# Kernel tuning notes

Hardware: AMD Instinct MI355X
Metric: run time of the kernel (lower is better)

The kernel has to match this reference:

```python
import jax, jax.numpy as jnp
import numpy as np

# ---- static architecture config (mirrors DynamicNetwork/MixedBlock) ----
B = 8192          # batch
ND = 13           # num dense feats
NS = 26           # num sparse feats
D = 16            # embedding_dim
VPF = 50000       # vocab per sparse field
VOCAB = ND + NS * VPF
BIN = 400         # block_in_dim
BOUT = 400        # block_out_dim
NB = 4            # num blocks
K = 4             # num candidate block types
REG = 1e-5        # weights_reg
# binarized one-hot arch choices (weights.data one-hot per segment in original)
CH1 = [0, 1, 1, 1]        # chosen prev node for input 1 of block i
CH2 = [1, 2, 3, 4]        # chosen prev node for input 2 of block i
CHK = [i % K for i in range(NB)]  # chosen candidate block type
OFFS = ND + VPF * np.arange(NS, dtype=np.int64)  # sparse field offsets


def _one_hot_alpha(n_prev, i1, i2, k):
    a = np.zeros(2 * n_prev + K, dtype=np.float32)
    a[i1] = 1.0
    a[n_prev + i2] = 1.0
    a[2 * n_prev + k] = 1.0
    return jnp.asarray(a)


def setup_inputs() -> dict:
    key = jax.random.key(0)
    ks = jax.random.split(key, 12)
    raw_dense = jax.random.uniform(ks[0], (B, ND), dtype=jnp.float32)
    raw_sparse = jax.random.randint(ks[1], (B, NS), 0, VPF, dtype=jnp.int64)
    emb_table = jax.random.normal(ks[2], (VOCAB, D), dtype=jnp.float32) * 0.01
    P_dense = jax.random.normal(ks[3], (ND * D, BIN), dtype=jnp.float32) * 0.02
    P_sparse = jax.random.normal(ks[4], (NS * D, BIN), dtype=jnp.float32) * 0.02
    P_block = jax.random.normal(ks[5], (BOUT, BIN), dtype=jnp.float32) * 0.02
    Wc = jax.random.normal(ks[6], (NB, K, BIN, BOUT), dtype=jnp.float32) * 0.02
    bc = jnp.zeros((NB, K, BOUT), dtype=jnp.float32)
    clf_w = jax.random.normal(ks[7], (NB * BOUT, 1), dtype=jnp.float32) * 0.02
    clf_b = jnp.zeros((1,), dtype=jnp.float32)
    alphas = {f'a{i}': _one_hot_alpha(2 + i, CH1[i], CH2[i], CHK[i]) for i in range(NB)}
    return dict(raw_dense=raw_dense, raw_sparse=raw_sparse, emb_table=emb_table,
                P_dense=P_dense, P_sparse=P_sparse, P_block=P_block,
                Wc=Wc, bc=bc, clf_w=clf_w, clf_b=clf_b, **alphas)


def _forward(raw_dense, raw_sparse, emb_table, P_dense, P_sparse, P_block,
             Wc, bc, clf_w, clf_b, alphas):
    # init node 1: dense embedding scaled by raw dense values -> [B, ND*D]
    dense_emb = emb_table[:ND][None, :, :] * raw_dense[:, :, None]
    # init node 2: sparse embedding lookup with field offsets -> [B, NS*D]
    sparse_idx = raw_sparse + jnp.asarray(OFFS)[None, :]
    sparse_emb = emb_table[sparse_idx]
    nodes = [dense_emb.reshape(B, ND * D), sparse_emb.reshape(B, NS * D)]
    projs = [P_dense, P_sparse]
    norms = jnp.linalg.norm(dense_emb) + jnp.linalg.norm(sparse_emb)
    for i in range(NB):
        n_prev = 2 + i
        a = alphas[i]
        seg1, seg2, segc = a[:n_prev], a[n_prev:2 * n_prev], a[-K:]
        i1, i2, kk = CH1[i], CH2[i], CHK[i]
        # masked weighted sum: chosen node scaled by its (one) weight; zero
        # weights enter additively as scalars (faithful to `else w` branch)
        x1 = seg1[i1] * nodes[i1] + (seg1.sum() - seg1[i1])
        x2 = seg2[i2] * nodes[i2] + (seg2.sum() - seg2[i2])
        # candidate block (MLP): type-specific input projection + ReLU + linear
        h = jax.nn.relu(x1 @ projs[i1] + x2 @ projs[i2])  # [B, BIN]
        out_k = h @ Wc[i, kk] + bc[i, kk]                 # [B, BOUT]
        node = segc[kk] * out_k + (segc.sum() - segc[kk])
        nodes.append(node)
        projs.append(P_block)
    output = jnp.concatenate(nodes[2:], axis=1)  # [B, NB*BOUT]
    logits = output @ clf_w + clf_b              # [B, 1]
    regs = REG * norms
    return logits, regs


def reference(raw_dense, raw_sparse, emb_table, P_dense, P_sparse, P_block,
              Wc, bc, clf_w, clf_b, a0, a1, a2, a3):
    return _forward(raw_dense, raw_sparse, emb_table, P_dense, P_sparse,
                    P_block, Wc, bc, clf_w, clf_b, [a0, a1, a2, a3])
```

## Files before the change

### kernel.cpp

```cpp
#include <hip/hip_runtime.h>
#include <cstddef>


typedef short short8 __attribute__((ext_vector_type(8)));
typedef float floatx16 __attribute__((ext_vector_type(16)));

#define EMB_BLOCKS 832

__device__ __forceinline__ unsigned short f2bf(float f) {
    unsigned int u = __float_as_uint(f);
    u += 0x7fffu + ((u >> 16) & 1u);
    return (unsigned short)(u >> 16);
}
__device__ __forceinline__ float bf2f(unsigned short h) {
    return __uint_as_float((unsigned int)h << 16);
}
__device__ __forceinline__ void split2(float v, unsigned short& h, unsigned short& l) {
    h = f2bf(v);
    l = f2bf(v - bf2f(h));
}

__global__ __launch_bounds__(256) void prep1_kernel(
    const float* __restrict__ Pd, const float* __restrict__ Ps, const float* __restrict__ Pb,
    const float* __restrict__ a0, const float* __restrict__ a1,
    const float* __restrict__ a2, const float* __restrict__ a3,
    float* __restrict__ scal,
    float* __restrict__ csd, float* __restrict__ css, float* __restrict__ csb)
{
    int t = threadIdx.x;
    int y = blockIdx.y;
    int c = t & 31, rg = t >> 5;
    int col = blockIdx.x * 32 + c;
    const float* src = (y==0) ? Pd : (y==1) ? Ps : Pb;
    int K = (y==0) ? 208 : (y==1) ? 416 : 400;
    float* out = (y==0) ? csd : (y==1) ? css : csb;
    float s = 0.f;
    if (col < 400)
        for (int k = rg; k < K; k += 8) s += src[(size_t)k*400 + col];
    __shared__ float red[8][32];
    red[rg][c] = s;
    __syncthreads();
    if (rg == 0 && col < 400) {
        float tot = 0.f;
        #pragma unroll
        for (int r = 0; r < 8; ++r) tot += red[r][c];
        out[col] = tot;
    }
    if (blockIdx.x == 0 && y == 0 && t < 4) {
        int i = t;
        const float* a = (i==0) ? a0 : (i==1) ? a1 : (i==2) ? a2 : a3;
        int np = 2 + i;
        float sum1 = 0.f, sum2 = 0.f, sumc = 0.f;
        for (int j = 0; j < np; ++j) { sum1 += a[j]; sum2 += a[np+j]; }
        for (int j = 0; j < 4; ++j) sumc += a[2*np+j];
        int i1 = (i==0) ? 0 : 1;
        int i2 = i + 1;
        int kk = i;
        float s1 = a[i1],      c1 = sum1 - s1;
        float s2 = a[np+i2],   c2 = sum2 - s2;
        float sk = a[2*np+kk], ck = sumc - sk;
        float* sl = scal + i*8;
        if (i == 0) { sl[0]=s1; sl[1]=c1; sl[2]=s2; sl[3]=c2; }
        else        { sl[0]=s2; sl[1]=c2; sl[2]=s1; sl[3]=c1; }
        sl[4] = sk; sl[5] = ck;
    }
}

__global__ __launch_bounds__(256) void prep2_kernel(
    const float* __restrict__ Pd, const float* __restrict__ Ps,
    const float* __restrict__ scal,
    unsigned short* __restrict__ w0, unsigned short* __restrict__ ws)
{
    int z = blockIdx.z;
    int Kp = (z==0) ? 208 : 416;
    const float* src = (z==0) ? Pd : Ps;
    unsigned short* dst = (z==0) ? w0 : ws;
    size_t plo = (size_t)512 * Kp;

    int ktiles = (Kp + 63) >> 6;
    if ((int)blockIdx.y >= ktiles) return;
    float sc = (z==0) ? scal[0] : 1.f;
    int k0 = blockIdx.y * 64, n0 = blockIdx.x * 64;
    __shared__ float T[64][65];
    int t = threadIdx.x;
    {
        int kr = t >> 2, c0 = (t & 3) * 16;
        int gk = k0 + kr;
        bool kok = gk < Kp;
        for (int j = 0; j < 16; j += 4) {
            int n = n0 + c0 + j;
            float4 v = make_float4(0.f,0.f,0.f,0.f);
            if (kok && n < 400) v = *(const float4*)&src[(size_t)gk*400 + n];
            T[kr][c0+j+0] = v.x * sc;
            T[kr][c0+j+1] = v.y * sc;
            T[kr][c0+j+2] = v.z * sc;
            T[kr][c0+j+3] = v.w * sc;
        }
    }
    __syncthreads();
    {
        int nr = t >> 2, kc0 = (t & 3) * 16;
        int gn = n0 + nr;
        int gk0 = k0 + kc0;
        if (gk0 >= Kp) return;
        unsigned short hb[16], lb[16];
        for (int j = 0; j < 16; ++j) {
            float v = (gn < 400) ? T[kc0+j][nr] : 0.f;
            split2(v, hb[j], lb[j]);
        }
        int kb = gk0 >> 4;
        size_t off = (((size_t)kb*16 + (gn>>5))*64 + (gn&31))*8;
        *(uint4*)&dst[off]             = *(uint4*)&hb[0];
        *(uint4*)&dst[off + 256]       = *(uint4*)&hb[8];
        *(uint4*)&dst[plo + off]       = *(uint4*)&lb[0];
        *(uint4*)&dst[plo + off + 256] = *(uint4*)&lb[8];
    }
}

__global__ __launch_bounds__(256) void prepM_kernel(
    const float* __restrict__ Wc, const float* __restrict__ Pb,
    const float* __restrict__ scal,
    unsigned short* __restrict__ w1, unsigned short* __restrict__ w2,
    unsigned short* __restrict__ w3)
{
    int z = blockIdx.z;
    unsigned short* dst = (z==0) ? w1 : (z==1) ? w2 : w3;
    const float* A = Wc + (size_t)z*5*160000;
    float scale = scal[(z+1)*8+0] * scal[z*8+4];
    const size_t plo = (size_t)512*400;

    __shared__ float As[16][68];
    __shared__ float Ws[16][68];
    int t = threadIdx.x;
    int tx = t & 15, ty = t >> 4;
    int bk = blockIdx.y * 64;
    int bn = blockIdx.x * 64;
    int arow = t >> 2;
    int aj4  = (t & 3) << 2;
    int wrow = t >> 4;
    int wc4  = (t & 15) << 2;
    float acc[4][4] = {};
    for (int j0 = 0; j0 < 400; j0 += 16) {
        float4 av = make_float4(0.f,0.f,0.f,0.f);
        if (bk + arow < 400) av = *(const float4*)&A[(size_t)(bk+arow)*400 + j0 + aj4];
        float4 wv = make_float4(0.f,0.f,0.f,0.f);
        if (bn + wc4 < 400) wv = *(const float4*)&Pb[(size_t)(j0+wrow)*400 + bn + wc4];
        __syncthreads();
        As[aj4+0][arow] = av.x;
        As[aj4+1][arow] = av.y;
        As[aj4+2][arow] = av.z;
        As[aj4+3][arow] = av.w;
        *(float4*)&Ws[wrow][wc4] = wv;
        __syncthreads();
        #pragma unroll
        for (int jj = 0; jj < 16; ++jj) {
            float4 a4 = *(const float4*)&As[jj][ty<<2];
            float4 b4 = *(const float4*)&Ws[jj][tx<<2];
            acc[0][0] += a4.x*b4.x; acc[0][1] += a4.x*b4.y; acc[0][2] += a4.x*b4.z; acc[0][3] += a4.x*b4.w;
            acc[1][0] += a4.y*b4.x; acc[1][1] += a4.y*b4.y; acc[1][2] += a4.y*b4.z; acc[1][3] += a4.y*b4.w;
            acc[2][0] += a4.z*b4.x; acc[2][1] += a4.z*b4.y; acc[2][2] += a4.z*b4.z; acc[2][3] += a4.z*b4.w;
            acc[3][0] += a4.w*b4.x; acc[3][1] += a4.w*b4.y; acc[3][2] += a4.w*b4.z; acc[3][3] += a4.w*b4.w;
        }
    }
    int gk0 = bk + (ty << 2);
    int gn0 = bn + (tx << 2);
    #pragma unroll
    for (int ik = 0; ik < 4; ++ik) {
        int gk = gk0 + ik;
        if (gk >= 400) break;
        int kb = gk >> 4, hh8 = (gk >> 3) & 1, e = gk & 7;
        #pragma unroll
        for (int in = 0; in < 4; ++in) {
            int gn = gn0 + in;
            float v = (gn < 400) ? acc[ik][in] * scale : 0.f;
            unsigned short h16, l16; split2(v, h16, l16);
            size_t off = (((size_t)kb*16 + (gn>>5))*64 + hh8*32 + (gn&31))*8 + e;
            dst[off] = h16;
            dst[plo + off] = l16;
        }
    }
}

__global__ __launch_bounds__(256) void prepvec_kernel(
    const float* __restrict__ scal,
    const float* __restrict__ csd, const float* __restrict__ css, const float* __restrict__ csb,
    const float* __restrict__ Wc, const float* __restrict__ bc,
    const float* __restrict__ clf_w, const float* __restrict__ Pb,
    float* __restrict__ cv, float* __restrict__ gv, float* __restrict__ scl2)
{
    int i = blockIdx.y;
    int tid = threadIdx.x;
    int tbase = blockIdx.x * 32;
    const float* cw = clf_w + i*400;
    float ski = scal[i*8+4], cki = scal[i*8+5];
    const float* A = Wc + (size_t)i*5*160000;

    int wv = tid >> 6, lane = tid & 63;
    #pragma unroll
    for (int q = 0; q < 8; ++q) {
        int t = tbase + wv*8 + q;
        float s = 0.f;
        if (t < 400) {
            const float* wr = A + (size_t)t*400;
            for (int j = lane; j < 400; j += 64) s += wr[j]*cw[j];
            #pragma unroll
            for (int o = 32; o > 0; o >>= 1) s += __shfl_xor(s, o);
        }
        if (lane == 0) gv[i*448 + t] = (t < 400) ? ski * s : 0.f;
    }

    __shared__ float bpred[8][32];
    int t = tbase + (tid & 31);
    int jc = tid >> 5;
    float bp_part = 0.f;
    if (i > 0 && t < 400) {
        const float* bcp = bc + (size_t)(i-1)*5*400;
        for (int j = jc*50; j < jc*50 + 50; ++j)
            bp_part += bcp[j] * Pb[(size_t)j*400 + t];
    }
    bpred[jc][tid & 31] = bp_part;
    __syncthreads();
    if (tid < 32) {
        float bp = 0.f;
        #pragma unroll
        for (int r = 0; r < 8; ++r) bp += bpred[r][tid];
        float c = 0.f;
        if (t < 400) {
            if (i == 0) {
                c = scal[1]*csd[t] + scal[3]*css[t];
            } else {
                float s2 = scal[i*8+0], c2 = scal[i*8+1];
                float c1 = scal[i*8+3];
                float skp = scal[(i-1)*8+4], ckp = scal[(i-1)*8+5];
                c = c1*css[t] + (c2 + s2*ckp)*csb[t] + s2*skp*bp;
            }
        }
        cv[i*448 + t] = c;
    }

    if (blockIdx.x == 0) {
        const float* bci = bc + (size_t)i*5*400;
        float sc = 0.f;
        for (int j = tid; j < 400; j += 256) sc += (ski*bci[j] + cki)*cw[j];
        #pragma unroll
        for (int o = 32; o > 0; o >>= 1) sc += __shfl_down(sc, o);
        __shared__ float red[4];
        int wv2 = tid >> 6, ln = tid & 63;
        if (ln == 0) red[wv2] = sc;
        __syncthreads();
        if (tid == 0) scl2[i] = red[0]+red[1]+red[2]+red[3];
    }
}

__global__ __launch_bounds__(256) void embed_kernel(
    const float* __restrict__ rd, const int* __restrict__ rs,
    const float* __restrict__ emb,
    unsigned short* __restrict__ n0h, unsigned short* __restrict__ n0l,
    unsigned short* __restrict__ n1h, unsigned short* __restrict__ n1l,
    float* __restrict__ partial)
{
    int tid0 = blockIdx.x*256 + threadIdx.x;
    int nth = gridDim.x*256;
    float ssq = 0.f, dsq = 0.f;
    for (int it = tid0; it < 8192*26; it += nth) {
        int s = it >> 13, b = it & 8191;
        int row = 13 + 50000*s + rs[b*26 + s];
        const float* e = emb + (size_t)row*16;
        float4 e0 = *(const float4*)&e[0], e1 = *(const float4*)&e[4];
        float4 e2 = *(const float4*)&e[8], e3 = *(const float4*)&e[12];
        float vv[16] = {e0.x,e0.y,e0.z,e0.w, e1.x,e1.y,e1.z,e1.w,
                        e2.x,e2.y,e2.z,e2.w, e3.x,e3.y,e3.z,e3.w};
        unsigned short hb[16], lb[16];
        for (int j = 0; j < 16; ++j) { ssq += vv[j]*vv[j]; split2(vv[j], hb[j], lb[j]); }
        size_t off = (((size_t)(b>>5)*26 + s)*64 + (b&31))*8;
        *(uint4*)&n1h[off]       = *(uint4*)&hb[0];
        *(uint4*)&n1h[off + 256] = *(uint4*)&hb[8];
        *(uint4*)&n1l[off]       = *(uint4*)&lb[0];
        *(uint4*)&n1l[off + 256] = *(uint4*)&lb[8];
    }
    for (int it = tid0; it < 8192*13; it += nth) {
        int f = it >> 13, b = it & 8191;
        float sc = rd[b*13 + f];
        const float* e = emb + (size_t)f*16;
        float4 e0 = *(const float4*)&e[0], e1 = *(const float4*)&e[4];
        float4 e2 = *(const float4*)&e[8], e3 = *(const float4*)&e[12];
        float vv[16] = {e0.x,e0.y,e0.z,e0.w, e1.x,e1.y,e1.z,e1.w,
                        e2.x,e2.y,e2.z,e2.w, e3.x,e3.y,e3.z,e3.w};
        unsigned short hb[16], lb[16];
        for (int j = 0; j < 16; ++j) { float v = vv[j]*sc; dsq += v*v; split2(v, hb[j], lb[j]); }
        size_t off = (((size_t)(b>>5)*13 + f)*64 + (b&31))*8;
        *(uint4*)&n0h[off]       = *(uint4*)&hb[0];
        *(uint4*)&n0h[off + 256] = *(uint4*)&hb[8];
        *(uint4*)&n0l[off]       = *(uint4*)&lb[0];
        *(uint4*)&n0l[off + 256] = *(uint4*)&lb[8];
    }
    for (int o = 32; o > 0; o >>= 1) { ssq += __shfl_down(ssq, o); dsq += __shfl_down(dsq, o); }
    __shared__ float red[8];
    int wave = threadIdx.x >> 6, lane = threadIdx.x & 63;
    if (lane == 0) { red[wave] = dsq; red[4+wave] = ssq; }
    __syncthreads();
    if (threadIdx.x == 0) {
        partial[blockIdx.x*2]   = red[0]+red[1]+red[2]+red[3];
        partial[blockIdx.x*2+1] = red[4]+red[5]+red[6]+red[7];
    }
}

__global__ __launch_bounds__(256) void finalize_kernel(
    const float* __restrict__ clf_b, const float* __restrict__ partial,
    const float* __restrict__ scl2, float* __restrict__ out)
{
    if (blockIdx.x < 32) {
        float base = clf_b[0] + scl2[0] + scl2[1] + scl2[2] + scl2[3];
        out[blockIdx.x*256 + threadIdx.x] = base;
        return;
    }
    float d = 0.f, s = 0.f;
    for (int i = threadIdx.x; i < EMB_BLOCKS; i += 256) { d += partial[2*i]; s += partial[2*i+1]; }
    for (int o = 32; o > 0; o >>= 1) { d += __shfl_down(d, o); s += __shfl_down(s, o); }
    __shared__ float red[8];
    int wave = threadIdx.x >> 6, lane = threadIdx.x & 63;
    if (lane == 0) { red[wave] = d; red[4+wave] = s; }
    __syncthreads();
    if (threadIdx.x == 0) {
        float dd = red[0]+red[1]+red[2]+red[3];
        float ss = red[4]+red[5]+red[6]+red[7];
        out[8192] = 1e-5f * (sqrtf(dd) + sqrtf(ss));
    }
}

#define MFMA_STEP(AH, AL, B0H, B1H, B0L, B1L, ACC0, ACC1)                      \
    ACC0 = __builtin_amdgcn_mfma_f32_32x32x16_bf16(AH, B0H, ACC0,0,0,0);       \
    ACC1 = __builtin_amdgcn_mfma_f32_32x32x16_bf16(AH, B1H, ACC1,0,0,0);       \
    ACC0 = __builtin_amdgcn_mfma_f32_32x32x16_bf16(AH, B0L, ACC0,0,0,0);       \
    ACC1 = __builtin_amdgcn_mfma_f32_32x32x16_bf16(AH, B1L, ACC1,0,0,0);       \
    ACC0 = __builtin_amdgcn_mfma_f32_32x32x16_bf16(AL, B0H, ACC0,0,0,0);       \
    ACC1 = __builtin_amdgcn_mfma_f32_32x32x16_bf16(AL, B1H, ACC1,0,0,0);

__global__ __launch_bounds__(448, 2) void fused_chain(
    const unsigned short* __restrict__ n0h, const unsigned short* __restrict__ n0l,
    const unsigned short* __restrict__ n1h, const unsigned short* __restrict__ n1l,
    const unsigned short* __restrict__ ws,
    const unsigned short* __restrict__ w0,
    const unsigned short* __restrict__ w1,
    const unsigned short* __restrict__ w2,
    const unsigned short* __restrict__ w3,
    const float* __restrict__ scal,
    const float* __restrict__ cv, const float* __restrict__ gv,
    float* __restrict__ out)
{
    __shared__ __align__(16) unsigned short hbuf[2][32][408];

    int tid = threadIdx.x;
    int W = tid >> 6, lane = tid & 63;
    int r31 = lane & 31, hh = lane >> 5;
    int mtile = blockIdx.x;
    int bm = mtile * 32;

    int gn0 = W*64 + r31;
    int gn1 = gn0 + 32;
    bool ok0 = gn0 < 400, ok1 = gn1 < 400;

    floatx16 p1a, p1b, acc0, acc1;
    float lrow[16];
    #pragma unroll
    for (int i = 0; i < 16; ++i) { p1a[i]=0.f; p1b[i]=0.f; lrow[i]=0.f; }

    {
        const unsigned short* Ah  = n1h + ((size_t)mtile*26*64 + lane)*8;
        const unsigned short* Al  = n1l + ((size_t)mtile*26*64 + lane)*8;
        const unsigned short* B0h = ws + ((size_t)(2*W)*64 + lane)*8;
        const unsigned short* B1h = ws + ((size_t)(2*W+1)*64 + lane)*8;
        const unsigned short* B0l = B0h + (size_t)512*416;
        const unsigned short* B1l = B1h + (size_t)512*416;
        #pragma unroll
        for (int k = 0; k < 26; ++k) {
            short8 ah  = *(const short8*)(Ah  + k*512);
            short8 al  = *(const short8*)(Al  + k*512);
            short8 b0h = *(const short8*)(B0h + k*8192);
            short8 b1h = *(const short8*)(B1h + k*8192);
            short8 b0l = *(const short8*)(B0l + k*8192);
            short8 b1l = *(const short8*)(B1l + k*8192);
            MFMA_STEP(ah, al, b0h, b1h, b0l, b1l, p1a, p1b)
        }
    }

    #define H_EPILOGUE(IVEC, FS, WRITE_H)                                      \
    do {                                                                       \
        const float* cvi = cv + (IVEC)*448;                                    \
        const float* gvi = gv + (IVEC)*448;                                    \
        float vc0 = ok0 ? cvi[gn0] : 0.f;                                      \
        float vc1 = ok1 ? cvi[gn1] : 0.f;                                      \
        float wv0 = ok0 ? gvi[gn0] : 0.f;                                      \
        float wv1 = ok1 ? gvi[gn1] : 0.f;                                      \
        _Pragma("unroll")                                                      \
        for (int j = 0; j < 16; ++j) {                                         \
            int row = (j & 3) + 8*(j >> 2) + 4*hh;                             \
            float v0 = acc0[j] + vc0 + (FS)*p1a[j];                            \
            float v1 = acc1[j] + vc1 + (FS)*p1b[j];                            \
            v0 = fmaxf(v0, 0.f); v1 = fmaxf(v1, 0.f);                          \
            lrow[j] += v0*wv0 + v1*wv1;                                        \
            if (WRITE_H) {                                                     \
                unsigned short h16, l16;                                       \
                if (ok0) { split2(v0, h16, l16);                               \
                    hbuf[0][row][gn0] = h16; hbuf[1][row][gn0] = l16; }        \
                if (ok1) { split2(v1, h16, l16);                               \
                    hbuf[0][row][gn1] = h16; hbuf[1][row][gn1] = l16; }        \
            }                                                                  \
        }                                                                      \
    } while (0)

    #pragma unroll
    for (int i = 0; i < 16; ++i) { acc0[i]=0.f; acc1[i]=0.f; }
    {
        const unsigned short* Ah  = n0h + ((size_t)mtile*13*64 + lane)*8;
        const unsigned short* Al  = n0l + ((size_t)mtile*13*64 + lane)*8;
        const unsigned short* B0h = w0 + ((size_t)(2*W)*64 + lane)*8;
        const unsigned short* B1h = w0 + ((size_t)(2*W+1)*64 + lane)*8;
        const unsigned short* B0l = B0h + (size_t)512*208;
        const unsigned short* B1l = B1h + (size_t)512*208;
        #pragma unroll
        for (int k = 0; k < 13; ++k) {
            short8 ah  = *(const short8*)(Ah  + k*512);
            short8 al  = *(const short8*)(Al  + k*512);
            short8 b0h = *(const short8*)(B0h + k*8192);
            short8 b1h = *(const short8*)(B1h + k*8192);
            short8 b0l = *(const short8*)(B0l + k*8192);
            short8 b1l = *(const short8*)(B1l + k*8192);
            MFMA_STEP(ah, al, b0h, b1h, b0l, b1l, acc0, acc1)
        }
    }
    float fs0 = scal[2];
    H_EPILOGUE(0, fs0, true);
    __syncthreads();

    #define H_STAGE_LDS(WPTR, IVEC, FS, WRITE_H, LAST)                         \
    do {                                                                       \
        _Pragma("unroll")                                                      \
        for (int i = 0; i < 16; ++i) { acc0[i]=0.f; acc1[i]=0.f; }             \
        const unsigned short* fAh = &hbuf[0][r31][hh*8];                       \
        const unsigned short* fAl = &hbuf[1][r31][hh*8];                       \
        const unsigned short* B0h = (WPTR) + ((size_t)(2*W)*64 + lane)*8;      \
        const unsigned short* B1h = (WPTR) + ((size_t)(2*W+1)*64 + lane)*8;    \
        const unsigned short* B0l = B0h + (size_t)512*400;                     \
        const unsigned short* B1l = B1h + (size_t)512*400;                     \
        _Pragma("unroll")                                                      \
        for (int k = 0; k < 25; ++k) {                                         \
            short8 ah  = *(const short8*)(fAh + k*16);                         \
            short8 al  = *(const short8*)(fAl + k*16);                         \
            short8 b0h = *(const short8*)(B0h + k*8192);                       \
            short8 b1h = *(const short8*)(B1h + k*8192);                       \
            short8 b0l = *(const short8*)(B0l + k*8192);                       \
            short8 b1l = *(const short8*)(B1l + k*8192);                       \
            MFMA_STEP(ah, al, b0h, b1h, b0l, b1l, acc0, acc1)                  \
        }                                                                      \
        if (!(LAST)) __syncthreads();       \
        H_EPILOGUE(IVEC, FS, WRITE_H);                                         \
        if (WRITE_H) __syncthreads();        \
    } while (0)

    float fs1 = scal[8+2], fs2 = scal[16+2], fs3 = scal[24+2];
    H_STAGE_LDS(w1, 1, fs1, true,  false);
    H_STAGE_LDS(w2, 2, fs2, true,  false);
    H_STAGE_LDS(w3, 3, fs3, false, true);

    #undef H_STAGE_LDS
    #undef H_EPILOGUE

    #pragma unroll
    for (int j = 0; j < 16; ++j) {
        float lv = lrow[j];
        #pragma unroll
        for (int o = 1; o < 32; o <<= 1) lv += __shfl_xor(lv, o);
        if (r31 == 0) {
            int row = (j & 3) + 8*(j >> 2) + 4*hh;
            atomicAdd(&out[bm + row], lv);
        }
    }
}

static inline size_t align64(size_t x) { return (x + 63) & ~(size_t)63; }

extern "C" void kernel_launch(void* const* d_in, const int* in_sizes, int n_in,
                              void* d_out, int out_size, void* d_ws, size_t ws_size,
                              hipStream_t stream)
{
    const float* raw_dense  = (const float*)d_in[0];
    const int*   raw_sparse = (const int*)d_in[1];
    const float* emb   = (const float*)d_in[2];
    const float* Pd    = (const float*)d_in[3];
    const float* Ps    = (const float*)d_in[4];
    const float* Pb    = (const float*)d_in[5];
    const float* Wc    = (const float*)d_in[6];
    const float* bc    = (const float*)d_in[7];
    const float* clf_w = (const float*)d_in[8];
    const float* clf_b = (const float*)d_in[9];
    const float* a0 = (const float*)d_in[10];
    const float* a1 = (const float*)d_in[11];
    const float* a2 = (const float*)d_in[12];
    const float* a3 = (const float*)d_in[13];
    float* out = (float*)d_out;

    char* p = (char*)d_ws;
    auto alloc = [&](size_t bytes) { char* r = p; p += align64(bytes); return r; };

    float* scal    = (float*)alloc(32*4);
    float* partial = (float*)alloc(2*EMB_BLOCKS*4);
    float* csd     = (float*)alloc(400*4);
    float* css     = (float*)alloc(400*4);
    float* csb     = (float*)alloc(400*4);
    float* cv      = (float*)alloc(4*448*4);
    float* gv      = (float*)alloc(4*448*4);
    float* scl2    = (float*)alloc(16*4);
    unsigned short* w0 = (unsigned short*)alloc((size_t)2*512*208*2);
    unsigned short* w1 = (unsigned short*)alloc((size_t)2*512*400*2);
    unsigned short* w2 = (unsigned short*)alloc((size_t)2*512*400*2);
    unsigned short* w3 = (unsigned short*)alloc((size_t)2*512*400*2);
    unsigned short* ws = (unsigned short*)alloc((size_t)2*512*416*2);
    unsigned short* n0h = (unsigned short*)alloc((size_t)256*13*512*2);
    unsigned short* n0l = (unsigned short*)alloc((size_t)256*13*512*2);
    unsigned short* n1h = (unsigned short*)alloc((size_t)256*26*512*2);
    unsigned short* n1l = (unsigned short*)alloc((size_t)256*26*512*2);

    prep1_kernel<<<dim3(13,3),256,0,stream>>>(Pd,Ps,Pb,a0,a1,a2,a3,scal,csd,css,csb);
    embed_kernel<<<EMB_BLOCKS,256,0,stream>>>(raw_dense, raw_sparse, emb, n0h,n0l,n1h,n1l, partial);
    prepM_kernel<<<dim3(8,7,3),256,0,stream>>>(Wc,Pb,scal,w1,w2,w3);
    prep2_kernel<<<dim3(8,7,2),256,0,stream>>>(Pd,Ps,scal,w0,ws);
    prepvec_kernel<<<dim3(14,4),256,0,stream>>>(scal,csd,css,csb,Wc,bc,clf_w,Pb,cv,gv,scl2);
    finalize_kernel<<<33,256,0,stream>>>(clf_b, partial, scl2, out);

    fused_chain<<<256,448,0,stream>>>(n0h,n0l,n1h,n1l, ws,w0,w1,w2,w3,
                                      scal, cv, gv, out);
}
```

Before: 315.6 us.

## Merge prep kernels into one launch and split-K the fused chain across warps

Four preprocessing kernels (embedding gather, column sums, weight transposition/splitting and the Wc·Pb product) are merged into one kernel that dispatches on block index. Scale factors are read straight from the alpha inputs instead of from the scal buffer, which removes a dependency between launches. The fused chain kernel doubles its thread count to 896 and splits each K-reduction between two wave groups that merge partial accumulators through shared memory. This is meant to cut launch overhead and add latency hiding in the MFMA chain, at the cost of extra shared-memory traffic, more barriers and higher register/LDS pressure per block.

```diff
diff --git a/kernel.cpp b/kernel.cpp
--- a/kernel.cpp
+++ b/kernel.cpp
@@ -20,163 +20,219 @@
     l = f2bf(v - bf2f(h));
 }
 
-__global__ __launch_bounds__(256) void prep1_kernel(
+__global__ __launch_bounds__(256) void mega_prep(
+    const float* __restrict__ rd, const int* __restrict__ rs,
+    const float* __restrict__ emb,
     const float* __restrict__ Pd, const float* __restrict__ Ps, const float* __restrict__ Pb,
+    const float* __restrict__ Wc,
     const float* __restrict__ a0, const float* __restrict__ a1,
     const float* __restrict__ a2, const float* __restrict__ a3,
     float* __restrict__ scal,
-    float* __restrict__ csd, float* __restrict__ css, float* __restrict__ csb)
+    float* __restrict__ csd, float* __restrict__ css, float* __restrict__ csb,
+    unsigned short* __restrict__ w0, unsigned short* __restrict__ ws,
+    unsigned short* __restrict__ w1, unsigned short* __restrict__ w2,
+    unsigned short* __restrict__ w3,
+    unsigned short* __restrict__ n0h, unsigned short* __restrict__ n0l,
+    unsigned short* __restrict__ n1h, unsigned short* __restrict__ n1l,
+    float* __restrict__ partial)
 {
+    __shared__ __align__(16) float smem[64*65];
+    int bid = blockIdx.x;
     int t = threadIdx.x;
-    int y = blockIdx.y;
-    int c = t & 31, rg = t >> 5;
-    int col = blockIdx.x * 32 + c;
-    const float* src = (y==0) ? Pd : (y==1) ? Ps : Pb;
-    int K = (y==0) ? 208 : (y==1) ? 416 : 400;
-    float* out = (y==0) ? csd : (y==1) ? css : csb;
-    float s = 0.f;
-    if (col < 400)
-        for (int k = rg; k < K; k += 8) s += src[(size_t)k*400 + col];
-    __shared__ float red[8][32];
-    red[rg][c] = s;
-    __syncthreads();
-    if (rg == 0 && col < 400) {
-        float tot = 0.f;
+
+    if (bid < 832) {
+        int tid0 = bid*256 + t;
+        const int nth = 832*256;
+        float ssq = 0.f, dsq = 0.f;
+        for (int it = tid0; it < 8192*26; it += nth) {
+            int s = it >> 13, b = it & 8191;
+            int row = 13 + 50000*s + rs[b*26 + s];
+            const float* e = emb + (size_t)row*16;
+            float4 e0 = *(const float4*)&e[0], e1 = *(const float4*)&e[4];
+            float4 e2 = *(const float4*)&e[8], e3 = *(const float4*)&e[12];
+            float vv[16] = {e0.x,e0.y,e0.z,e0.w, e1.x,e1.y,e1.z,e1.w,
+                            e2.x,e2.y,e2.z,e2.w, e3.x,e3.y,e3.z,e3.w};
+            unsigned short hb[16], lb[16];
+            for (int j = 0; j < 16; ++j) { ssq += vv[j]*vv[j]; split2(vv[j], hb[j], lb[j]); }
+            size_t off = (((size_t)(b>>5)*26 + s)*64 + (b&31))*8;
+            *(uint4*)&n1h[off]       = *(uint4*)&hb[0];
+            *(uint4*)&n1h[off + 256] = *(uint4*)&hb[8];
+            *(uint4*)&n1l[off]       = *(uint4*)&lb[0];
+            *(uint4*)&n1l[off + 256] = *(uint4*)&lb[8];
+        }
+        for (int it = tid0; it < 8192*13; it += nth) {
+            int f = it >> 13, b = it & 8191;
+            float sc = rd[b*13 + f];
+            const float* e = emb + (size_t)f*16;
+            float4 e0 = *(const float4*)&e[0], e1 = *(const float4*)&e[4];
+            float4 e2 = *(const float4*)&e[8], e3 = *(const float4*)&e[12];
+            float vv[16] = {e0.x,e0.y,e0.z,e0.w, e1.x,e1.y,e1.z,e1.w,
+                            e2.x,e2.y,e2.z,e2.w, e3.x,e3.y,e3.z,e3.w};
+            unsigned short hb[16], lb[16];
+            for (int j = 0; j < 16; ++j) { float v = vv[j]*sc; dsq += v*v; split2(v, hb[j], lb[j]); }
+            size_t off = (((size_t)(b>>5)*13 + f)*64 + (b&31))*8;
+            *(uint4*)&n0h[off]       = *(uint4*)&hb[0];
+            *(uint4*)&n0h[off + 256] = *(uint4*)&hb[8];
+            *(uint4*)&n0l[off]       = *(uint4*)&lb[0];
+            *(uint4*)&n0l[off + 256] = *(uint4*)&lb[8];
+        }
+        for (int o = 32; o > 0; o >>= 1) { ssq += __shfl_down(ssq, o); dsq += __shfl_down(dsq, o); }
+        float* red = smem;
+        int wave = t >> 6, lane = t & 63;
+        if (lane == 0) { red[wave] = dsq; red[4+wave] = ssq; }
+        __syncthreads();
+        if (t == 0) {
+            partial[bid*2]   = red[0]+red[1]+red[2]+red[3];
+            partial[bid*2+1] = red[4]+red[5]+red[6]+red[7];
+        }
+        return;
+    }
+    if (bid < 871) {
+        int r = bid - 832;
+        int x = r % 13, y = r / 13;
+        int c = t & 31, rg = t >> 5;
+        int col = x * 32 + c;
+        const float* src = (y==0) ? Pd : (y==1) ? Ps : Pb;
+        int K = (y==0) ? 208 : (y==1) ? 416 : 400;
+        float* outp = (y==0) ? csd : (y==1) ? css : csb;
+        float s = 0.f;
+        if (col < 400)
+            for (int k = rg; k < K; k += 8) s += src[(size_t)k*400 + col];
+        float (*red)[32] = (float(*)[32])smem;
+        red[rg][c] = s;
+        __syncthreads();
+        if (rg == 0 && col < 400) {
+            float tot = 0.f;
+            #pragma unroll
+            for (int rr = 0; rr < 8; ++rr) tot += red[rr][c];
+            outp[col] = tot;
+        }
+        if (x == 0 && y == 0 && t < 4) {
+            int i = t;
+            const float* a = (i==0) ? a0 : (i==1) ? a1 : (i==2) ? a2 : a3;
+            int np = 2 + i;
+            float sum1 = 0.f, sum2 = 0.f, sumc = 0.f;
+            for (int j = 0; j < np; ++j) { sum1 += a[j]; sum2 += a[np+j]; }
+            for (int j = 0; j < 4; ++j) sumc += a[2*np+j];
+            int i1 = (i==0) ? 0 : 1;
+            int i2 = i + 1;
+            int kk = i;
+            float s1 = a[i1],      c1 = sum1 - s1;
+            float s2 = a[np+i2],   c2 = sum2 - s2;
+            float sk = a[2*np+kk], ck = sumc - sk;
+            float* sl = scal + i*8;
+            if (i == 0) { sl[0]=s1; sl[1]=c1; sl[2]=s2; sl[3]=c2; }
+            else        { sl[0]=s2; sl[1]=c2; sl[2]=s1; sl[3]=c1; }
+            sl[4] = sk; sl[5] = ck;
+        }
+        return;
+    }
+    if (bid < 983) {
+        int r = bid - 871;
+        int z = r / 56, rem = r % 56;
+        int y = rem / 8, x = rem % 8;
+        int Kp = (z==0) ? 208 : 416;
+        const float* src = (z==0) ? Pd : Ps;
+        unsigned short* dst = (z==0) ? w0 : ws;
+        size_t plo = (size_t)512 * Kp;
+        int ktiles = (Kp + 63) >> 6;
+        if (y >= ktiles) return;
+        float sc = (z==0) ? a0[0] : 1.f;
+        int k0 = y * 64, n0 = x * 64;
+        float (*T)[65] = (float(*)[65])smem;
+        {
+            int kr = t >> 2, c0 = (t & 3) * 16;
+            int gk = k0 + kr;
+            bool kok = gk < Kp;
+            for (int j = 0; j < 16; j += 4) {
+                int n = n0 + c0 + j;
+                float4 v = make_float4(0.f,0.f,0.f,0.f);
+                if (kok && n < 400) v = *(const float4*)&src[(size_t)gk*400 + n];
+                T[kr][c0+j+0] = v.x * sc;
+                T[kr][c0+j+1] = v.y * sc;
+                T[kr][c0+j+2] = v.z * sc;
+                T[kr][c0+j+3] = v.w * sc;
+            }
+        }
+        __syncthreads();
+        {
+            int nr = t >> 2, kc0 = (t & 3) * 16;
+            int gn = n0 + nr;
+            int gk0 = k0 + kc0;
+            if (gk0 >= Kp) return;
+            unsigned short hb[16], lb[16];
+            for (int j = 0; j < 16; ++j) {
+                float v = (gn < 400) ? T[kc0+j][nr] : 0.f;
+                split2(v, hb[j], lb[j]);
+            }
+            int kb = gk0 >> 4;
+            size_t off = (((size_t)kb*16 + (gn>>5))*64 + (gn&31))*8;
+            *(uint4*)&dst[off]             = *(uint4*)&hb[0];
+            *(uint4*)&dst[off + 256]       = *(uint4*)&hb[8];
+            *(uint4*)&dst[plo + off]       = *(uint4*)&lb[0];
+            *(uint4*)&dst[plo + off + 256] = *(uint4*)&lb[8];
+        }
+        return;
+    }
+    {
+        int r = bid - 983;
+        int z = r / 56, rem = r % 56;
+        int by = rem / 8, bx = rem % 8;
+        unsigned short* dst = (z==0) ? w1 : (z==1) ? w2 : w3;
+        const float* A = Wc + (size_t)z*5*160000;
+        const float* az1 = (z==0) ? a1 : (z==1) ? a2 : a3;
+        const float* az  = (z==0) ? a0 : (z==1) ? a1 : a2;
+        float scale = az1[2*z+5] * az[3*z+4];
+        const size_t plo = (size_t)512*400;
+
+        float (*As)[68] = (float(*)[68])smem;
+        float (*Ws)[68] = (float(*)[68])(smem + 16*68);
+        int tx = t & 15, ty = t >> 4;
+        int bk = by * 64;
+        int bn = bx * 64;
+        int arow = t >> 2;
+        int aj4  = (t & 3) << 2;
+        int wrow = t >> 4;
+        int wc4  = (t & 15) << 2;
+        float acc[4][4] = {};
+        for (int j0 = 0; j0 < 400; j0 += 16) {
+            float4 av = make_float4(0.f,0.f,0.f,0.f);
+            if (bk + arow < 400) av = *(const float4*)&A[(size_t)(bk+arow)*400 + j0 + aj4];
+            float4 wv = make_float4(0.f,0.f,0.f,0.f);
+            if (bn + wc4 < 400) wv = *(const float4*)&Pb[(size_t)(j0+wrow)*400 + bn + wc4];
+            __syncthreads();
+            As[aj4+0][arow] = av.x;
+            As[aj4+1][arow] = av.y;
+            As[aj4+2][arow] = av.z;
+            As[aj4+3][arow] = av.w;
+            *(float4*)&Ws[wrow][wc4] = wv;
+            __syncthreads();
+            #pragma unroll
+            for (int jj = 0; jj < 16; ++jj) {
+                float4 a4 = *(const float4*)&As[jj][ty<<2];
+                float4 b4 = *(const float4*)&Ws[jj][tx<<2];
+                acc[0][0] += a4.x*b4.x; acc[0][1] += a4.x*b4.y; acc[0][2] += a4.x*b4.z; acc[0][3] += a4.x*b4.w;
+                acc[1][0] += a4.y*b4.x; acc[1][1] += a4.y*b4.y; acc[1][2] += a4.y*b4.z; acc[1][3] += a4.y*b4.w;
+                acc[2][0] += a4.z*b4.x; acc[2][1] += a4.z*b4.y; acc[2][2] += a4.z*b4.z; acc[2][3] += a4.z*b4.w;
+                acc[3][0] += a4.w*b4.x; acc[3][1] += a4.w*b4.y; acc[3][2] += a4.w*b4.z; acc[3][3] += a4.w*b4.w;
+            }
+        }
+        int gk0 = bk + (ty << 2);
+        int gn0 = bn + (tx << 2);
         #pragma unroll
-        for (int r = 0; r < 8; ++r) tot += red[r][c];
-        out[col] = tot;
-    }
-    if (blockIdx.x == 0 && y == 0 && t < 4) {
-        int i = t;
-        const float* a = (i==0) ? a0 : (i==1) ? a1 : (i==2) ? a2 : a3;
-        int np = 2 + i;
-        float sum1 = 0.f, sum2 = 0.f, sumc = 0.f;
-        for (int j = 0; j < np; ++j) { sum1 += a[j]; sum2 += a[np+j]; }
-        for (int j = 0; j < 4; ++j) sumc += a[2*np+j];
-        int i1 = (i==0) ? 0 : 1;
-        int i2 = i + 1;
-        int kk = i;
-        float s1 = a[i1],      c1 = sum1 - s1;
-        float s2 = a[np+i2],   c2 = sum2 - s2;
-        float sk = a[2*np+kk], ck = sumc - sk;
-        float* sl = scal + i*8;
-        if (i == 0) { sl[0]=s1; sl[1]=c1; sl[2]=s2; sl[3]=c2; }
-        else        { sl[0]=s2; sl[1]=c2; sl[2]=s1; sl[3]=c1; }
-        sl[4] = sk; sl[5] = ck;
-    }
-}
-
-__global__ __launch_bounds__(256) void prep2_kernel(
-    const float* __restrict__ Pd, const float* __restrict__ Ps,
-    const float* __restrict__ scal,
-    unsigned short* __restrict__ w0, unsigned short* __restrict__ ws)
-{
-    int z = blockIdx.z;
-    int Kp = (z==0) ? 208 : 416;
-    const float* src = (z==0) ? Pd : Ps;
-    unsigned short* dst = (z==0) ? w0 : ws;
-    size_t plo = (size_t)512 * Kp;
-
-    int ktiles = (Kp + 63) >> 6;
-    if ((int)blockIdx.y >= ktiles) return;
-    float sc = (z==0) ? scal[0] : 1.f;
-    int k0 = blockIdx.y * 64, n0 = blockIdx.x * 64;
-    __shared__ float T[64][65];
-    int t = threadIdx.x;
-    {
-        int kr = t >> 2, c0 = (t & 3) * 16;
-        int gk = k0 + kr;
-        bool kok = gk < Kp;
-        for (int j = 0; j < 16; j += 4) {
-            int n = n0 + c0 + j;
-            float4 v = make_float4(0.f,0.f,0.f,0.f);
-            if (kok && n < 400) v = *(const float4*)&src[(size_t)gk*400 + n];
-            T[kr][c0+j+0] = v.x * sc;
-            T[kr][c0+j+1] = v.y * sc;
-            T[kr][c0+j+2] = v.z * sc;
-            T[kr][c0+j+3] = v.w * sc;
-        }
-    }
-    __syncthreads();
-    {
-        int nr = t >> 2, kc0 = (t & 3) * 16;
-        int gn = n0 + nr;
-        int gk0 = k0 + kc0;
-        if (gk0 >= Kp) return;
-        unsigned short hb[16], lb[16];
-        for (int j = 0; j < 16; ++j) {
-            float v = (gn < 400) ? T[kc0+j][nr] : 0.f;
-            split2(v, hb[j], lb[j]);
-        }
-        int kb = gk0 >> 4;
-        size_t off = (((size_t)kb*16 + (gn>>5))*64 + (gn&31))*8;
-        *(uint4*)&dst[off]             = *(uint4*)&hb[0];
-        *(uint4*)&dst[off + 256]       = *(uint4*)&hb[8];
-        *(uint4*)&dst[plo + off]       = *(uint4*)&lb[0];
-        *(uint4*)&dst[plo + off + 256] = *(uint4*)&lb[8];
-    }
-}
-
-__global__ __launch_bounds__(256) void prepM_kernel(
-    const float* __restrict__ Wc, const float* __restrict__ Pb,
-    const float* __restrict__ scal,
-    unsigned short* __restrict__ w1, unsigned short* __restrict__ w2,
-    unsigned short* __restrict__ w3)
-{
-    int z = blockIdx.z;
-    unsigned short* dst = (z==0) ? w1 : (z==1) ? w2 : w3;
-    const float* A = Wc + (size_t)z*5*160000;
-    float scale = scal[(z+1)*8+0] * scal[z*8+4];
-    const size_t plo = (size_t)512*400;
-
-    __shared__ float As[16][68];
-    __shared__ float Ws[16][68];
-    int t = threadIdx.x;
-    int tx = t & 15, ty = t >> 4;
-    int bk = blockIdx.y * 64;
-    int bn = blockIdx.x * 64;
-    int arow = t >> 2;
-    int aj4  = (t & 3) << 2;
-    int wrow = t >> 4;
-    int wc4  = (t & 15) << 2;
-    float acc[4][4] = {};
-    for (int j0 = 0; j0 < 400; j0 += 16) {
-        float4 av = make_float4(0.f,0.f,0.f,0.f);
-        if (bk + arow < 400) av = *(const float4*)&A[(size_t)(bk+arow)*400 + j0 + aj4];
-        float4 wv = make_float4(0.f,0.f,0.f,0.f);
-        if (bn + wc4 < 400) wv = *(const float4*)&Pb[(size_t)(j0+wrow)*400 + bn + wc4];
-        __syncthreads();
-        As[aj4+0][arow] = av.x;
-        As[aj4+1][arow] = av.y;
-        As[aj4+2][arow] = av.z;
-        As[aj4+3][arow] = av.w;
-        *(float4*)&Ws[wrow][wc4] = wv;
-        __syncthreads();
-        #pragma unroll
-        for (int jj = 0; jj < 16; ++jj) {
-            float4 a4 = *(const float4*)&As[jj][ty<<2];
-            float4 b4 = *(const float4*)&Ws[jj][tx<<2];
-            acc[0][0] += a4.x*b4.x; acc[0][1] += a4.x*b4.y; acc[0][2] += a4.x*b4.z; acc[0][3] += a4.x*b4.w;
-            acc[1][0] += a4.y*b4.x; acc[1][1] += a4.y*b4.y; acc[1][2] += a4.y*b4.z; acc[1][3] += a4.y*b4.w;
-            acc[2][0] += a4.z*b4.x; acc[2][1] += a4.z*b4.y; acc[2][2] += a4.z*b4.z; acc[2][3] += a4.z*b4.w;
-            acc[3][0] += a4.w*b4.x; acc[3][1] += a4.w*b4.y; acc[3][2] += a4.w*b4.z; acc[3][3] += a4.w*b4.w;
-        }
-    }
-    int gk0 = bk + (ty << 2);
-    int gn0 = bn + (tx << 2);
-    #pragma unroll
-    for (int ik = 0; ik < 4; ++ik) {
-        int gk = gk0 + ik;
-        if (gk >= 400) break;
-        int kb = gk >> 4, hh8 = (gk >> 3) & 1, e = gk & 7;
-        #pragma unroll
-        for (int in = 0; in < 4; ++in) {
-            int gn = gn0 + in;
-            float v = (gn < 400) ? acc[ik][in] * scale : 0.f;
-            unsigned short h16, l16; split2(v, h16, l16);
-            size_t off = (((size_t)kb*16 + (gn>>5))*64 + hh8*32 + (gn&31))*8 + e;
-            dst[off] = h16;
-            dst[plo + off] = l16;
+        for (int ik = 0; ik < 4; ++ik) {
+            int gk = gk0 + ik;
+            if (gk >= 400) break;
+            int kb = gk >> 4, hh8 = (gk >> 3) & 1, e = gk & 7;
+            #pragma unroll
+            for (int in = 0; in < 4; ++in) {
+                int gn = gn0 + in;
+                float v = (gn < 400) ? acc[ik][in] * scale : 0.f;
+                unsigned short h16, l16; split2(v, h16, l16);
+                size_t off = (((size_t)kb*16 + (gn>>5))*64 + hh8*32 + (gn&31))*8 + e;
+                dst[off] = h16;
+                dst[plo + off] = l16;
+            }
         }
     }
 }
@@ -252,59 +308,6 @@
     }
 }
 
-__global__ __launch_bounds__(256) void embed_kernel(
-    const float* __restrict__ rd, const int* __restrict__ rs,
-    const float* __restrict__ emb,
-    unsigned short* __restrict__ n0h, unsigned short* __restrict__ n0l,
-    unsigned short* __restrict__ n1h, unsigned short* __restrict__ n1l,
-    float* __restrict__ partial)
-{
-    int tid0 = blockIdx.x*256 + threadIdx.x;
-    int nth = gridDim.x*256;
-    float ssq = 0.f, dsq = 0.f;
-    for (int it = tid0; it < 8192*26; it += nth) {
-        int s = it >> 13, b = it & 8191;
-        int row = 13 + 50000*s + rs[b*26 + s];
-        const float* e = emb + (size_t)row*16;
-        float4 e0 = *(const float4*)&e[0], e1 = *(const float4*)&e[4];
-        float4 e2 = *(const float4*)&e[8], e3 = *(const float4*)&e[12];
-        float vv[16] = {e0.x,e0.y,e0.z,e0.w, e1.x,e1.y,e1.z,e1.w,
-                        e2.x,e2.y,e2.z,e2.w, e3.x,e3.y,e3.z,e3.w};
-        unsigned short hb[16], lb[16];
-        for (int j = 0; j < 16; ++j) { ssq += vv[j]*vv[j]; split2(vv[j], hb[j], lb[j]); }
-        size_t off = (((size_t)(b>>5)*26 + s)*64 + (b&31))*8;
-        *(uint4*)&n1h[off]       = *(uint4*)&hb[0];
-        *(uint4*)&n1h[off + 256] = *(uint4*)&hb[8];
-        *(uint4*)&n1l[off]       = *(uint4*)&lb[0];
-        *(uint4*)&n1l[off + 256] = *(uint4*)&lb[8];
-    }
-    for (int it = tid0; it < 8192*13; it += nth) {
-        int f = it >> 13, b = it & 8191;
-        float sc = rd[b*13 + f];
-        const float* e = emb + (size_t)f*16;
-        float4 e0 = *(const float4*)&e[0], e1 = *(const float4*)&e[4];
-        float4 e2 = *(const float4*)&e[8], e3 = *(const float4*)&e[12];
-        float vv[16] = {e0.x,e0.y,e0.z,e0.w, e1.x,e1.y,e1.z,e1.w,
-                        e2.x,e2.y,e2.z,e2.w, e3.x,e3.y,e3.z,e3.w};
-        unsigned short hb[16], lb[16];
-        for (int j = 0; j < 16; ++j) { float v = vv[j]*sc; dsq += v*v; split2(v, hb[j], lb[j]); }
-        size_t off = (((size_t)(b>>5)*13 + f)*64 + (b&31))*8;
-        *(uint4*)&n0h[off]       = *(uint4*)&hb[0];
-        *(uint4*)&n0h[off + 256] = *(uint4*)&hb[8];
-        *(uint4*)&n0l[off]       = *(uint4*)&lb[0];
-        *(uint4*)&n0l[off + 256] = *(uint4*)&lb[8];
-    }
-    for (int o = 32; o > 0; o >>= 1) { ssq += __shfl_down(ssq, o); dsq += __shfl_down(dsq, o); }
-    __shared__ float red[8];
-    int wave = threadIdx.x >> 6, lane = threadIdx.x & 63;
-    if (lane == 0) { red[wave] = dsq; red[4+wave] = ssq; }
-    __syncthreads();
-    if (threadIdx.x == 0) {
-        partial[blockIdx.x*2]   = red[0]+red[1]+red[2]+red[3];
-        partial[blockIdx.x*2+1] = red[4]+red[5]+red[6]+red[7];
-    }
-}
-
 __global__ __launch_bounds__(256) void finalize_kernel(
     const float* __restrict__ clf_b, const float* __restrict__ partial,
     const float* __restrict__ scl2, float* __restrict__ out)
@@ -336,7 +339,7 @@
     ACC0 = __builtin_amdgcn_mfma_f32_32x32x16_bf16(AL, B0H, ACC0,0,0,0);       \
     ACC1 = __builtin_amdgcn_mfma_f32_32x32x16_bf16(AL, B1H, ACC1,0,0,0);
 
-__global__ __launch_bounds__(448, 2) void fused_chain(
+__global__ __launch_bounds__(896, 4) void fused_chain(
     const unsigned short* __restrict__ n0h, const unsigned short* __restrict__ n0l,
     const unsigned short* __restrict__ n1h, const unsigned short* __restrict__ n1l,
     const unsigned short* __restrict__ ws,
@@ -349,14 +352,16 @@
     float* __restrict__ out)
 {
     __shared__ __align__(16) unsigned short hbuf[2][32][408];
+    __shared__ __align__(16) float pbuf[14][64][16];
 
     int tid = threadIdx.x;
     int W = tid >> 6, lane = tid & 63;
     int r31 = lane & 31, hh = lane >> 5;
+    int c = W % 7, kw = W / 7;
     int mtile = blockIdx.x;
     int bm = mtile * 32;
 
-    int gn0 = W*64 + r31;
+    int gn0 = c*64 + r31;
     int gn1 = gn0 + 32;
     bool ok0 = gn0 < 400, ok1 = gn1 < 400;
 
@@ -365,24 +370,48 @@
     #pragma unroll
     for (int i = 0; i < 16; ++i) { p1a[i]=0.f; p1b[i]=0.f; lrow[i]=0.f; }
 
+    #define PBUF_WRITE(V0, V1)                                                 \
+    do {                                                                       \
+        _Pragma("unroll")                                                      \
+        for (int j4 = 0; j4 < 4; ++j4) {                                       \
+            *(float4*)&pbuf[2*c  ][lane][j4*4] =                               \
+                make_float4(V0[j4*4+0],V0[j4*4+1],V0[j4*4+2],V0[j4*4+3]);      \
+            *(float4*)&pbuf[2*c+1][lane][j4*4] =                               \
+                make_float4(V1[j4*4+0],V1[j4*4+1],V1[j4*4+2],V1[j4*4+3]);      \
+        }                                                                      \
+    } while (0)
+
+    #define PBUF_MERGE(V0, V1)                                                 \
+    do {                                                                       \
+        _Pragma("unroll")                                                      \
+        for (int j = 0; j < 16; ++j) {                                         \
+            V0[j] += pbuf[2*c][lane][j];                                       \
+            V1[j] += pbuf[2*c+1][lane][j];                                     \
+        }                                                                      \
+    } while (0)
+
     {
-        const unsigned short* Ah  = n1h + ((size_t)mtile*26*64 + lane)*8;
-        const unsigned short* Al  = n1l + ((size_t)mtile*26*64 + lane)*8;
-        const unsigned short* B0h = ws + ((size_t)(2*W)*64 + lane)*8;
-        const unsigned short* B1h = ws + ((size_t)(2*W+1)*64 + lane)*8;
+        const unsigned short* Ah  = n1h + ((size_t)mtile*26*64 + lane)*8 + kw*512;
+        const unsigned short* Al  = n1l + ((size_t)mtile*26*64 + lane)*8 + kw*512;
+        const unsigned short* B0h = ws + ((size_t)(2*c)*64 + lane)*8 + (size_t)kw*8192;
+        const unsigned short* B1h = ws + ((size_t)(2*c+1)*64 + lane)*8 + (size_t)kw*8192;
         const unsigned short* B0l = B0h + (size_t)512*416;
         const unsigned short* B1l = B1h + (size_t)512*416;
         #pragma unroll
-        for (int k = 0; k < 26; ++k) {
-            short8 ah  = *(const short8*)(Ah  + k*512);
-            short8 al  = *(const short8*)(Al  + k*512);
-            short8 b0h = *(const short8*)(B0h + k*8192);
-            short8 b1h = *(const short8*)(B1h + k*8192);
-            short8 b0l = *(const short8*)(B0l + k*8192);
-            short8 b1l = *(const short8*)(B1l + k*8192);
+        for (int kq = 0; kq < 13; ++kq) {
+            short8 ah  = *(const short8*)(Ah  + kq*1024);
+            short8 al  = *(const short8*)(Al  + kq*1024);
+            short8 b0h = *(const short8*)(B0h + kq*16384);
+            short8 b1h = *(const short8*)(B1h + kq*16384);
+            short8 b0l = *(const short8*)(B0l + kq*16384);
+            short8 b1l = *(const short8*)(B1l + kq*16384);
             MFMA_STEP(ah, al, b0h, b1h, b0l, b1l, p1a, p1b)
         }
     }
+    if (kw) PBUF_WRITE(p1a, p1b);
+    __syncthreads();
+    if (!kw) PBUF_MERGE(p1a, p1b);
+    __syncthreads();
 
     #define H_EPILOGUE(IVEC, FS, WRITE_H)                                      \
     do {                                                                       \
@@ -412,50 +441,55 @@
     #pragma unroll
     for (int i = 0; i < 16; ++i) { acc0[i]=0.f; acc1[i]=0.f; }
     {
-        const unsigned short* Ah  = n0h + ((size_t)mtile*13*64 + lane)*8;
-        const unsigned short* Al  = n0l + ((size_t)mtile*13*64 + lane)*8;
-        const unsigned short* B0h = w0 + ((size_t)(2*W)*64 + lane)*8;
-        const unsigned short* B1h = w0 + ((size_t)(2*W+1)*64 + lane)*8;
+        const unsigned short* Ah  = n0h + ((size_t)mtile*13*64 + lane)*8 + kw*512;
+        const unsigned short* Al  = n0l + ((size_t)mtile*13*64 + lane)*8 + kw*512;
+        const unsigned short* B0h = w0 + ((size_t)(2*c)*64 + lane)*8 + (size_t)kw*8192;
+        const unsigned short* B1h = w0 + ((size_t)(2*c+1)*64 + lane)*8 + (size_t)kw*8192;
         const unsigned short* B0l = B0h + (size_t)512*208;
         const unsigned short* B1l = B1h + (size_t)512*208;
         #pragma unroll
-        for (int k = 0; k < 13; ++k) {
-            short8 ah  = *(const short8*)(Ah  + k*512);
-            short8 al  = *(const short8*)(Al  + k*512);
-            short8 b0h = *(const short8*)(B0h + k*8192);
-            short8 b1h = *(const short8*)(B1h + k*8192);
-            short8 b0l = *(const short8*)(B0l + k*8192);
-            short8 b1l = *(const short8*)(B1l + k*8192);
+        for (int kq = 0; kq < 7; ++kq) {
+            if (kq == 6 && kw) break;
+            short8 ah  = *(const short8*)(Ah  + kq*1024);
+            short8 al  = *(const short8*)(Al  + kq*1024);
+            short8 b0h = *(const short8*)(B0h + kq*16384);
+            short8 b1h = *(const short8*)(B1h + kq*16384);
+            short8 b0l = *(const short8*)(B0l + kq*16384);
+            short8 b1l = *(const short8*)(B1l + kq*16384);
             MFMA_STEP(ah, al, b0h, b1h, b0l, b1l, acc0, acc1)
         }
     }
     float fs0 = scal[2];
-    H_EPILOGUE(0, fs0, true);
+    if (kw) PBUF_WRITE(acc0, acc1);
+    __syncthreads();
+    if (!kw) { PBUF_MERGE(acc0, acc1); H_EPILOGUE(0, fs0, true); }
     __syncthreads();
 
     #define H_STAGE_LDS(WPTR, IVEC, FS, WRITE_H, LAST)                         \
     do {                                                                       \
         _Pragma("unroll")                                                      \
         for (int i = 0; i < 16; ++i) { acc0[i]=0.f; acc1[i]=0.f; }             \
-        const unsigned short* fAh = &hbuf[0][r31][hh*8];                       \
-        const unsigned short* fAl = &hbuf[1][r31][hh*8];                       \
-        const unsigned short* B0h = (WPTR) + ((size_t)(2*W)*64 + lane)*8;      \
-        const unsigned short* B1h = (WPTR) + ((size_t)(2*W+1)*64 + lane)*8;    \
+        const unsigned short* fAh = &hbuf[0][r31][hh*8] + kw*16;               \
+        const unsigned short* fAl = &hbuf[1][r31][hh*8] + kw*16;               \
+        const unsigned short* B0h = (WPTR) + ((size_t)(2*c)*64 + lane)*8 + (size_t)kw*8192;   \
+        const unsigned short* B1h = (WPTR) + ((size_t)(2*c+1)*64 + lane)*8 + (size_t)kw*8192; \
         const unsigned short* B0l = B0h + (size_t)512*400;                     \
         const unsigned short* B1l = B1h + (size_t)512*400;                     \
         _Pragma("unroll")                                                      \
-        for (int k = 0; k < 25; ++k) {                                         \
-            short8 ah  = *(const short8*)(fAh + k*16);                         \
-            short8 al  = *(const short8*)(fAl + k*16);                         \
-            short8 b0h = *(const short8*)(B0h + k*8192);                       \
-            short8 b1h = *(const short8*)(B1h + k*8192);                       \
-            short8 b0l = *(const short8*)(B0l + k*8192);                       \
-            short8 b1l = *(const short8*)(B1l + k*8192);                       \
+        for (int kq = 0; kq < 13; ++kq) {                                      \
+            if (kq == 12 && kw) break;                                         \
+            short8 ah  = *(const short8*)(fAh + kq*32);                        \
+            short8 al  = *(const short8*)(fAl + kq*32);                        \
+            short8 b0h = *(const short8*)(B0h + kq*16384);                     \
+            short8 b1h = *(const short8*)(B1h + kq*16384);                     \
+            short8 b0l = *(const short8*)(B0l + kq*16384);                     \
+            short8 b1l = *(const short8*)(B1l + kq*16384);                     \
             MFMA_STEP(ah, al, b0h, b1h, b0l, b1l, acc0, acc1)                  \
         }                                                                      \
-        if (!(LAST)) __syncthreads();       \
-        H_EPILOGUE(IVEC, FS, WRITE_H);                                         \
-        if (WRITE_H) __syncthreads();        \
+        if (kw) PBUF_WRITE(acc0, acc1);                                       \
+        __syncthreads();                                                       \
+        if (!kw) { PBUF_MERGE(acc0, acc1); H_EPILOGUE(IVEC, FS, WRITE_H); }    \
+        if (!(LAST)) __syncthreads();                                          \
     } while (0)
 
     float fs1 = scal[8+2], fs2 = scal[16+2], fs3 = scal[24+2];
@@ -465,15 +499,19 @@
 
     #undef H_STAGE_LDS
     #undef H_EPILOGUE
-
-    #pragma unroll
-    for (int j = 0; j < 16; ++j) {
-        float lv = lrow[j];
+    #undef PBUF_WRITE
+    #undef PBUF_MERGE
+
+    if (!kw) {
         #pragma unroll
-        for (int o = 1; o < 32; o <<= 1) lv += __shfl_xor(lv, o);
-        if (r31 == 0) {
-            int row = (j & 3) + 8*(j >> 2) + 4*hh;
-            atomicAdd(&out[bm + row], lv);
+        for (int j = 0; j < 16; ++j) {
+            float lv = lrow[j];
+            #pragma unroll
+            for (int o = 1; o < 32; o <<= 1) lv += __shfl_xor(lv, o);
+            if (r31 == 0) {
+                int row = (j & 3) + 8*(j >> 2) + 4*hh;
+                atomicAdd(&out[bm + row], lv);
+            }
         }
     }
 }
@@ -521,13 +559,13 @@
     unsigned short* n1h = (unsigned short*)alloc((size_t)256*26*512*2);
     unsigned short* n1l = (unsigned short*)alloc((size_t)256*26*512*2);
 
-    prep1_kernel<<<dim3(13,3),256,0,stream>>>(Pd,Ps,Pb,a0,a1,a2,a3,scal,csd,css,csb);
-    embed_kernel<<<EMB_BLOCKS,256,0,stream>>>(raw_dense, raw_sparse, emb, n0h,n0l,n1h,n1l, partial);
-    prepM_kernel<<<dim3(8,7,3),256,0,stream>>>(Wc,Pb,scal,w1,w2,w3);
-    prep2_kernel<<<dim3(8,7,2),256,0,stream>>>(Pd,Ps,scal,w0,ws);
+    mega_prep<<<1151,256,0,stream>>>(raw_dense, raw_sparse, emb, Pd, Ps, Pb, Wc,
+                                     a0,a1,a2,a3, scal, csd,css,csb,
+                                     w0, ws, w1, w2, w3,
+                                     n0h,n0l,n1h,n1l, partial);
     prepvec_kernel<<<dim3(14,4),256,0,stream>>>(scal,csd,css,csb,Wc,bc,clf_w,Pb,cv,gv,scl2);
     finalize_kernel<<<33,256,0,stream>>>(clf_b, partial, scl2, out);
 
-    fused_chain<<<256,448,0,stream>>>(n0h,n0l,n1h,n1l, ws,w0,w1,w2,w3,
+    fused_chain<<<256,896,0,stream>>>(n0h,n0l,n1h,n1l, ws,w0,w1,w2,w3,
                                       scal, cv, gv, out);
 }
```

After: 263.5 us. -16.5%, faster.
